# Kernel tuning notes

Measured on AMD Instinct MI355X. Metric: run time of the kernel, lower is better.

The kernel has to match this reference:

```python
import jax, jax.numpy as jnp
import numpy as np

LN_EPS = 1e-5


def setup_inputs() -> dict:
    key = jax.random.key(0)
    ks = jax.random.split(key, 6)
    T, B, D, O, G = 32, 4096, 128, 128, 9
    x = jax.random.normal(ks[0], (T, B, D), dtype=jnp.float32)
    sequence_mask = jnp.ones((T, B, 1), dtype=bool)
    # freq: arange(1,G+1)/(G+1)  (norm_freq=True, is_first=False)
    freq = (jnp.arange(1, G + 1, dtype=jnp.float32) / (G + 1)).reshape(1, 1, 1, G)
    # phase buffer: grid_phase + input_phase + small perturbations
    grid_phase = jnp.linspace(0.0, np.pi, G).reshape(1, 1, 1, G)
    input_phase = jnp.linspace(0.0, np.pi, D).reshape(1, 1, D, 1)
    gp_pert = jax.random.uniform(ks[1], (1, 1, 1, G)) / G * 0.1
    ip_pert = jax.random.uniform(ks[2], (1, 1, D, 1)) / D * 0.1
    phase = (grid_phase + input_phase + gp_pert + ip_pert).astype(jnp.float32)
    # amplitudes: uniform(-1,1)/O / grid_norm_factor  -> (O, D, G)
    grid_norm = (jnp.arange(G, dtype=jnp.float32) + 1.0).reshape(1, 1, G)
    amplitudes = (jax.random.uniform(ks[3], (O, D, 1), minval=-1.0, maxval=1.0) / O) / grid_norm
    bias = jnp.ones((1, O), dtype=jnp.float32) / O
    ln_weight = jnp.ones((D,), dtype=jnp.float32)
    ln_bias = jnp.zeros((D,), dtype=jnp.float32)
    return {"x": x, "sequence_mask": sequence_mask, "freq": freq, "phase": phase,
            "amplitudes": amplitudes, "bias": bias, "ln_weight": ln_weight, "ln_bias": ln_bias}


def reference(x, sequence_mask, freq, phase, amplitudes, bias, ln_weight, ln_bias):
    T, B, D = x.shape
    O, _, G = amplitudes.shape
    # LayerNorm over feature dim
    mu = jnp.mean(x, axis=-1, keepdims=True)
    var = jnp.mean(jnp.square(x - mu), axis=-1, keepdims=True)
    xn = (x - mu) * jax.lax.rsqrt(var + LN_EPS) * ln_weight + ln_bias
    xf = xn.reshape(T * B, D)
    # sine basis expansion: (N, D, G)
    s = jnp.sin(xf[:, :, None] * freq.reshape(1, 1, G) + phase.reshape(1, D, G))
    # contraction to output dim: (N, O)
    y = jnp.einsum('nkg,okg->no', s, amplitudes) + bias
    y = y.reshape(T, B, O)
    return y * sequence_mask.astype(y.dtype)
```

## Files before the change

### kernel.cpp

```cpp
#include <hip/hip_runtime.h>
#include <hip/hip_bf16.h>

typedef __attribute__((ext_vector_type(8))) short short8;
typedef __attribute__((ext_vector_type(16))) float f32x16;
typedef __attribute__((ext_vector_type(4))) unsigned uint4v;
typedef unsigned int u32;

#define D_DIM 128
#define G_DIM 9
#define O_DIM 128
#define K_DIM 1152
#define BROWS 256
#define NTHR 512
#define INV2PI 0.15915494309189535f

__device__ __forceinline__ short f2bf(float f) {
  unsigned u = __float_as_uint(f);
  unsigned r = (u + 0x7FFFu + ((u >> 16) & 1u)) >> 16;
  return (short)r;
}

__device__ __forceinline__ unsigned pk2bf(float a, float b) {
  __hip_bfloat162 h = __float22bfloat162_rn(float2{a, b});
  return *reinterpret_cast<unsigned*>(&h);
}

__global__ void sinekan_prep(const float* __restrict__ amp,
                             const float* __restrict__ phase,
                             const float* __restrict__ freq,
                             short* __restrict__ Bp,
                             float* __restrict__ pt2,
                             float* __restrict__ fq2) {
  int i = blockIdx.x * blockDim.x + threadIdx.x;
  if (i < G_DIM * O_DIM * D_DIM) {
    int g = i >> 14, rem = i & 16383, o = rem >> 7, d = rem & 127;
    Bp[(g << 14) + (o << 7) + (d ^ ((o & 7) << 3))] = f2bf(amp[(o * D_DIM + d) * G_DIM + g]);
  }
  if (i < K_DIM) {
    int g = i >> 7, d = i & 127;
    pt2[i] = phase[d * G_DIM + g] * INV2PI;
  }
  if (i < G_DIM) fq2[i] = freq[i] * INV2PI;
}

__device__ __forceinline__ void stage_b(const short* __restrict__ Bp, short* dst_lds,
                                        int g, int tid) {
  const char* src = (const char*)Bp + ((size_t)g << 15) + tid * 16;
  char* dst = (char*)dst_lds + (tid >> 6) * 1024;
#pragma unroll
  for (int c = 0; c < 4; ++c) {
    __builtin_amdgcn_global_load_lds(
        (const __attribute__((address_space(1))) u32*)(src + c * 8192),
        (__attribute__((address_space(3))) u32*)(dst + c * 8192), 16, 0, 0);
  }
}

__global__ __launch_bounds__(NTHR, 3)
void sinekan_fused(const float* __restrict__ x,
                   const int* __restrict__ mask,
                   const float* __restrict__ bias,
                   const float* __restrict__ lnw,
                   const float* __restrict__ lnb,
                   const short* __restrict__ Bp,
                   const float* __restrict__ pt2,
                   const float* __restrict__ fq2,
                   float* __restrict__ out) {
  __shared__ short b_lds[2][O_DIM * D_DIM];
  __shared__ float pt_lds[G_DIM * D_DIM];
  __shared__ float mu_s[BROWS], rs_s[BROWS], mk_s[BROWS];
  __shared__ float w_s[D_DIM], bb_s[D_DIM];

  const int tid = threadIdx.x;
  const int row0 = blockIdx.x * BROWS;
  const int wv = tid >> 6, lane = tid & 63, lr = lane & 31, hi = lane >> 5;

  stage_b(Bp, b_lds[0], 0, tid);

  if (tid < D_DIM) { w_s[tid] = lnw[tid]; bb_s[tid] = lnb[tid]; }
  if (tid < BROWS) mk_s[tid] = mask[row0 + tid] ? 1.0f : 0.0f;
  for (int i = tid; i < G_DIM * D_DIM; i += NTHR) pt_lds[i] = pt2[i];

  {
    int rloc = tid >> 4, ch = tid & 15;
#pragma unroll 1
    for (int it = 0; it < 8; ++it) {
      int r = it * 32 + rloc;
      const float4* xp = (const float4*)(x + (size_t)(row0 + r) * D_DIM + ch * 8);
      float4 a = xp[0], b = xp[1];
      float s  = a.x + a.y + a.z + a.w + b.x + b.y + b.z + b.w;
      float sq = a.x*a.x + a.y*a.y + a.z*a.z + a.w*a.w
               + b.x*b.x + b.y*b.y + b.z*b.z + b.w*b.w;
#pragma unroll
      for (int off = 1; off < 16; off <<= 1) {
        s  += __shfl_xor(s, off, 64);
        sq += __shfl_xor(sq, off, 64);
      }
      if (ch == 0) {
        float m = s * (1.0f / 128.0f);
        mu_s[r] = m;
        rs_s[r] = rsqrtf(sq * (1.0f / 128.0f) - m * m + 1e-5f);
      }
    }
  }
  __syncthreads();

  uint4v xnc[8];
  {
    const int rl = wv * 32 + lr;
    const float mu = mu_s[rl], rs = rs_s[rl];
    const float* xr = x + (size_t)(row0 + rl) * D_DIM;
#pragma unroll
    for (int kk = 0; kk < 8; ++kk) {
      const int d0 = kk * 16 + hi * 8;
      float4 xa = *(const float4*)(xr + d0);
      float4 xb = *(const float4*)(xr + d0 + 4);
      float xv[8] = {xa.x, xa.y, xa.z, xa.w, xb.x, xb.y, xb.z, xb.w};
      uint4v pk;
#pragma unroll
      for (int jj = 0; jj < 4; ++jj) {
        float e0 = (xv[2*jj]   - mu) * rs * w_s[d0 + 2*jj]   + bb_s[d0 + 2*jj];
        float e1 = (xv[2*jj+1] - mu) * rs * w_s[d0 + 2*jj+1] + bb_s[d0 + 2*jj+1];
        pk[jj] = pk2bf(e0, e1);
      }
      xnc[kk] = pk;
    }
  }

  const int hs = (hi << 4) ^ ((lr & 7) << 4);
  const char* blr = (const char*)&b_lds[0][0] + (lr << 8);
  const float* ptl = pt_lds + (hi << 3);

  f32x16 acc[4] = {};

#pragma unroll 1
  for (int g = 0; g < G_DIM; ++g) {
    if (g + 1 < G_DIM) stage_b(Bp, b_lds[(g + 1) & 1], g + 1, tid);
    const float fgv = fq2[g];
    const char* bl = blr + ((g & 1) << 15);
    const float* ptg = ptl + (g << 7);

    float4 p0 = *(const float4*)(ptg);
    float4 p1 = *(const float4*)(ptg + 4);

#pragma unroll
    for (int kk = 0; kk < 8; ++kk) {
      const char* ba = bl + ((kk << 5) ^ hs);
      short8 bf0 = *(const short8*)(ba);
      short8 bf1 = *(const short8*)(ba + 8192);
      short8 bf2 = *(const short8*)(ba + 16384);
      short8 bf3 = *(const short8*)(ba + 24576);
      const int kn = (kk + 1) & 7;
      float4 q0 = *(const float4*)(ptg + kn * 16);
      float4 q1 = *(const float4*)(ptg + kn * 16 + 4);

      const float ph[8] = {p0.x, p0.y, p0.z, p0.w, p1.x, p1.y, p1.z, p1.w};
      uint4v pk;
#pragma unroll
      for (int jj = 0; jj < 4; ++jj) {
        unsigned u = xnc[kk][jj];
        float s0 = __builtin_amdgcn_sinf(fmaf(__uint_as_float(u << 16),         fgv, ph[2*jj]));
        float s1 = __builtin_amdgcn_sinf(fmaf(__uint_as_float(u & 0xffff0000u), fgv, ph[2*jj+1]));
        pk[jj] = pk2bf(s0, s1);
      }
      short8 af = __builtin_bit_cast(short8, pk);

      __builtin_amdgcn_s_setprio(1);
      acc[0] = __builtin_amdgcn_mfma_f32_32x32x16_bf16(af, bf0, acc[0], 0, 0, 0);
      acc[1] = __builtin_amdgcn_mfma_f32_32x32x16_bf16(af, bf1, acc[1], 0, 0, 0);
      acc[2] = __builtin_amdgcn_mfma_f32_32x32x16_bf16(af, bf2, acc[2], 0, 0, 0);
      acc[3] = __builtin_amdgcn_mfma_f32_32x32x16_bf16(af, bf3, acc[3], 0, 0, 0);
      __builtin_amdgcn_s_setprio(0);

      p0 = q0; p1 = q1;
    }
    __syncthreads();
  }

#pragma unroll
  for (int n = 0; n < 4; ++n) {
    int col = n * 32 + lr;
    float bv = bias[col];
#pragma unroll
    for (int reg = 0; reg < 16; ++reg) {
      int rit  = (reg & 3) + 8 * (reg >> 2) + 4 * hi;
      int rloc = wv * 32 + rit;
      out[(size_t)(row0 + rloc) * O_DIM + col] = (acc[n][reg] + bv) * mk_s[rloc];
    }
  }
}

extern "C" void kernel_launch(void* const* d_in, const int* in_sizes, int n_in,
                              void* d_out, int out_size, void* d_ws, size_t ws_size,
                              hipStream_t stream) {
  const float* x    = (const float*)d_in[0];
  const int* mk     = (const int*)d_in[1];
  const float* freq = (const float*)d_in[2];
  const float* phase= (const float*)d_in[3];
  const float* amp  = (const float*)d_in[4];
  const float* bias = (const float*)d_in[5];
  const float* lnw  = (const float*)d_in[6];
  const float* lnb  = (const float*)d_in[7];
  float* out = (float*)d_out;

  int N = in_sizes[0] / D_DIM;
  short* Bp = (short*)d_ws;
  float* pt2 = (float*)((char*)d_ws + (size_t)G_DIM * O_DIM * D_DIM * sizeof(short));
  float* fq2 = pt2 + G_DIM * D_DIM;

  int total = G_DIM * O_DIM * D_DIM;
  sinekan_prep<<<(total + 255) / 256, 256, 0, stream>>>(amp, phase, freq, Bp, pt2, fq2);
  sinekan_fused<<<N / BROWS, NTHR, 0, stream>>>(x, mk, bias, lnw, lnb, Bp, pt2, fq2, out);
}
```

Baseline: 184.4 us.

## Repack B into MFMA fragment order, prefetch B registers, keep normalized x in fp32

Changes the prep kernel to store the bf16 amplitude matrix in per-lane MFMA fragment order (kk, hi, o, j), so each lane reads contiguous 16-byte chunks without the XOR swizzle. The inner loop now double-buffers the B fragments in registers, loading the next kk's fragments before the current MFMAs are issued. Normalized x is kept in fp32 registers (64 floats) instead of packed bf16, which removes the unpack work and the bf16 rounding of x before the sine. The trade-off is much higher register pressure under launch_bounds(512,3), which risks spills or lower occupancy.

```diff
diff --git a/kernel.cpp b/kernel.cpp
--- a/kernel.cpp
+++ b/kernel.cpp
@@ -33,8 +33,16 @@
                              float* __restrict__ fq2) {
   int i = blockIdx.x * blockDim.x + threadIdx.x;
   if (i < G_DIM * O_DIM * D_DIM) {
-    int g = i >> 14, rem = i & 16383, o = rem >> 7, d = rem & 127;
-    Bp[(g << 14) + (o << 7) + (d ^ ((o & 7) << 3))] = f2bf(amp[(o * D_DIM + d) * G_DIM + g]);
+    int g    = i >> 14;
+    int rem  = i & 16383;
+    int kk   = rem >> 11;
+    int rem2 = rem & 2047;
+    int hi   = rem2 >> 10;
+    int rem3 = rem2 & 1023;
+    int o    = rem3 >> 3;
+    int j    = rem3 & 7;
+    int d    = kk * 16 + hi * 8 + j;
+    Bp[i] = f2bf(amp[(o * D_DIM + d) * G_DIM + g]);
   }
   if (i < K_DIM) {
     int g = i >> 7, d = i & 127;
@@ -104,7 +112,7 @@
   }
   __syncthreads();
 
-  uint4v xnc[8];
+  float xc[8][8];
   {
     const int rl = wv * 32 + lr;
     const float mu = mu_s[rl], rs = rs_s[rl];
@@ -115,19 +123,13 @@
       float4 xa = *(const float4*)(xr + d0);
       float4 xb = *(const float4*)(xr + d0 + 4);
       float xv[8] = {xa.x, xa.y, xa.z, xa.w, xb.x, xb.y, xb.z, xb.w};
-      uint4v pk;
-#pragma unroll
-      for (int jj = 0; jj < 4; ++jj) {
-        float e0 = (xv[2*jj]   - mu) * rs * w_s[d0 + 2*jj]   + bb_s[d0 + 2*jj];
-        float e1 = (xv[2*jj+1] - mu) * rs * w_s[d0 + 2*jj+1] + bb_s[d0 + 2*jj+1];
-        pk[jj] = pk2bf(e0, e1);
-      }
-      xnc[kk] = pk;
-    }
-  }
-
-  const int hs = (hi << 4) ^ ((lr & 7) << 4);
-  const char* blr = (const char*)&b_lds[0][0] + (lr << 8);
+#pragma unroll
+      for (int j = 0; j < 8; ++j)
+        xc[kk][j] = (xv[j] - mu) * rs * w_s[d0 + j] + bb_s[d0 + j];
+    }
+  }
+
+  const char* bbase = (const char*)&b_lds[0][0] + (hi << 11) + (lr << 4);
   const float* ptl = pt_lds + (hi << 3);
 
   f32x16 acc[4] = {};
@@ -136,39 +138,49 @@
   for (int g = 0; g < G_DIM; ++g) {
     if (g + 1 < G_DIM) stage_b(Bp, b_lds[(g + 1) & 1], g + 1, tid);
     const float fgv = fq2[g];
-    const char* bl = blr + ((g & 1) << 15);
+    const char* bl = bbase + ((g & 1) << 15);
     const float* ptg = ptl + (g << 7);
 
+    short8 bf[2][4];
     float4 p0 = *(const float4*)(ptg);
     float4 p1 = *(const float4*)(ptg + 4);
+    {
+      const char* ba = bl;
+      bf[0][0] = *(const short8*)(ba);
+      bf[0][1] = *(const short8*)(ba + 512);
+      bf[0][2] = *(const short8*)(ba + 1024);
+      bf[0][3] = *(const short8*)(ba + 1536);
+    }
 
 #pragma unroll
     for (int kk = 0; kk < 8; ++kk) {
-      const char* ba = bl + ((kk << 5) ^ hs);
-      short8 bf0 = *(const short8*)(ba);
-      short8 bf1 = *(const short8*)(ba + 8192);
-      short8 bf2 = *(const short8*)(ba + 16384);
-      short8 bf3 = *(const short8*)(ba + 24576);
-      const int kn = (kk + 1) & 7;
-      float4 q0 = *(const float4*)(ptg + kn * 16);
-      float4 q1 = *(const float4*)(ptg + kn * 16 + 4);
+      const int cur = kk & 1, nxt = cur ^ 1;
+      float4 q0 = p0, q1 = p1;
+      if (kk < 7) {
+        const char* bn = bl + ((kk + 1) << 12);
+        bf[nxt][0] = *(const short8*)(bn);
+        bf[nxt][1] = *(const short8*)(bn + 512);
+        bf[nxt][2] = *(const short8*)(bn + 1024);
+        bf[nxt][3] = *(const short8*)(bn + 1536);
+        q0 = *(const float4*)(ptg + (kk + 1) * 16);
+        q1 = *(const float4*)(ptg + (kk + 1) * 16 + 4);
+      }
 
       const float ph[8] = {p0.x, p0.y, p0.z, p0.w, p1.x, p1.y, p1.z, p1.w};
       uint4v pk;
 #pragma unroll
       for (int jj = 0; jj < 4; ++jj) {
-        unsigned u = xnc[kk][jj];
-        float s0 = __builtin_amdgcn_sinf(fmaf(__uint_as_float(u << 16),         fgv, ph[2*jj]));
-        float s1 = __builtin_amdgcn_sinf(fmaf(__uint_as_float(u & 0xffff0000u), fgv, ph[2*jj+1]));
+        float s0 = __builtin_amdgcn_sinf(fmaf(xc[kk][2*jj],     fgv, ph[2*jj]));
+        float s1 = __builtin_amdgcn_sinf(fmaf(xc[kk][2*jj + 1], fgv, ph[2*jj + 1]));
         pk[jj] = pk2bf(s0, s1);
       }
       short8 af = __builtin_bit_cast(short8, pk);
 
       __builtin_amdgcn_s_setprio(1);
-      acc[0] = __builtin_amdgcn_mfma_f32_32x32x16_bf16(af, bf0, acc[0], 0, 0, 0);
-      acc[1] = __builtin_amdgcn_mfma_f32_32x32x16_bf16(af, bf1, acc[1], 0, 0, 0);
-      acc[2] = __builtin_amdgcn_mfma_f32_32x32x16_bf16(af, bf2, acc[2], 0, 0, 0);
-      acc[3] = __builtin_amdgcn_mfma_f32_32x32x16_bf16(af, bf3, acc[3], 0, 0, 0);
+      acc[0] = __builtin_amdgcn_mfma_f32_32x32x16_bf16(af, bf[cur][0], acc[0], 0, 0, 0);
+      acc[1] = __builtin_amdgcn_mfma_f32_32x32x16_bf16(af, bf[cur][1], acc[1], 0, 0, 0);
+      acc[2] = __builtin_amdgcn_mfma_f32_32x32x16_bf16(af, bf[cur][2], acc[2], 0, 0, 0);
+      acc[3] = __builtin_amdgcn_mfma_f32_32x32x16_bf16(af, bf[cur][3], acc[3], 0, 0, 0);
       __builtin_amdgcn_s_setprio(0);
 
       p0 = q0; p1 = q1;
```

New measurement: 221.6 us. +20.2%, slower.
